# Optimization experiments

Hardware: AMD Instinct MI355X
Metric: run time of the kernel (lower is better)

## Reference

```python
import jax, jax.numpy as jnp
import numpy as np

# norse default LIFParameters (dt=1e-3): tau_mem_inv=100, tau_syn_inv=200, v_leak=0, v_reset=0
DT = 1e-3
TAU_MEM_INV = 100.0
TAU_SYN_INV = 200.0
V_TH_ENC = 1.0   # encoder built with default LIFParameters -> v_th=1.0
V_TH = 0.33      # LIF cells built with v_th=0.33
SEQ_LEN = 24
ALPHA = 100.0    # SuperSpike surrogate-gradient slope (norse 'super' method)

@jax.custom_vjp
def heaviside(x):
    # forward: hard threshold; backward: SuperSpike surrogate 1/(alpha*|x|+1)^2
    return (x > 0).astype(x.dtype)

def _hv_fwd(x):
    return heaviside(x), x

def _hv_bwd(x, g):
    return (g / (ALPHA * jnp.abs(x) + 1.0) ** 2,)

heaviside.defvjp(_hv_fwd, _hv_bwd)


def setup_inputs() -> dict:
    key = jax.random.key(0)
    ks = jax.random.split(key, 6)
    B, F, H, C = 4096, 1024, 256, 10
    def lin(k, fan_out, fan_in):  # torch Linear default init (no bias)
        bound = 1.0 / np.sqrt(fan_in)
        return jax.random.uniform(k, (fan_out, fan_in), jnp.float32, -bound, bound)
    return {
        "x": jax.random.normal(ks[0], (B, F), jnp.float32),
        "W1": lin(ks[1], H, F),
        "W2": lin(ks[2], H, H),
        "W3": lin(ks[3], H, H),
        "Wout": jax.random.normal(ks[4], (C, H), jnp.float32) * np.sqrt(2.0 / H),
        "feature_scalar": jnp.ones((1,), jnp.float32),
        "encoder_scalar": jnp.ones((1,), jnp.float32),
    }


def _lif_step(z_in, v, i):
    # norse lif_feed_forward_step: decay v/i from old state, spike, reset, then inject input into i
    v_dec = v + DT * TAU_MEM_INV * (-v + i)
    i_dec = i * (1.0 - DT * TAU_SYN_INV)
    z = heaviside(v_dec - V_TH)
    v_new = (1.0 - z) * v_dec  # v_reset = 0
    i_new = i_dec + z_in
    return z, v_new, i_new


def reference(x, W1, W2, W3, Wout, feature_scalar, encoder_scalar):
    B, F = x.shape
    H = W1.shape[0]
    C = Wout.shape[0]
    current = 2.0 * feature_scalar * x  # constant injected current, [B, F]
    z0 = lambda d: jnp.zeros((B, d), x.dtype)
    init = (z0(F), z0(H), z0(H), z0(H), z0(H), z0(H), z0(H), z0(C), z0(C))

    def step(state, _):
        v_enc, v1, i1, v2, i2, v3, i3, v_li, i_li = state
        # ConstantCurrentLIFEncoder (lif_current_encoder, v_th=1.0)
        v_enc = v_enc + DT * TAU_MEM_INV * (-v_enc + current)
        s = heaviside(v_enc - V_TH_ENC)
        v_enc = v_enc - s * v_enc  # reset to 0
        z = 5.0 * encoder_scalar * s
        # three Linear(no bias)+LIF stages (dropout in eval mode = identity)
        z, v1, i1 = _lif_step(1.2 * (z @ W1.T), v1, i1)
        z, v2, i2 = _lif_step(1.2 * (z @ W2.T), v2, i2)
        z, v3, i3 = _lif_step(1.2 * (z @ W3.T), v3, i3)
        # LILinearCell: leaky integrator readout
        v_li = v_li + DT * TAU_MEM_INV * (-v_li + i_li)
        i_li = i_li * (1.0 - DT * TAU_SYN_INV) + z @ Wout.T
        return (v_enc, v1, i1, v2, i2, v3, i3, v_li, i_li), None

    final, _ = jax.lax.scan(step, init, None, length=SEQ_LEN)
    return final[7]  # decode = voltages[-1], shape [B, n_classes]
```

## Files before the change

kernel.cpp:

```cpp
#include <hip/hip_runtime.h>

using u16 = unsigned short;
using u32 = unsigned int;
using u64 = unsigned long long;

typedef _Float16 half8 __attribute__((ext_vector_type(8)));
typedef float  f32x4 __attribute__((ext_vector_type(4)));
typedef u32    u32x4 __attribute__((ext_vector_type(4)));
typedef u32    u32x2 __attribute__((ext_vector_type(2)));

#define T_STEPS 24
#define NB 4096
#define NF 1024
#define NH 256
#define NCLS 10

static __device__ __forceinline__ void f16split(float w, u16& hi, u16& lo) {
  _Float16 h = (_Float16)w;
  float hf = (float)h;
  if (__builtin_fabsf(hf) < 6.103515625e-05f) { h = (_Float16)0.0f; hf = 0.0f; }
  float r = __fmul_rn(__fsub_rn(w, hf), 4096.0f);
  _Float16 l = (_Float16)r;
  hi = __builtin_bit_cast(u16, h);
  lo = __builtin_bit_cast(u16, l);
}

__global__ __launch_bounds__(256) void k_prep(const float* __restrict__ W1,
                                              const float* __restrict__ W2,
                                              const float* __restrict__ W3,
                                              u16* __restrict__ W1hl,
                                              u16* __restrict__ W2hl,
                                              u16* __restrict__ W3hl) {
  int blk = blockIdx.x, tid = threadIdx.x;
  const float* src; u16* dst; int K; int g;
  if (blk < 1024)      { src = W1; dst = W1hl; K = 1024; g = blk * 256 + tid; }
  else if (blk < 1280) { src = W2; dst = W2hl; K = 256;  g = (blk - 1024) * 256 + tid; }
  else                 { src = W3; dst = W3hl; K = 256;  g = (blk - 1280) * 256 + tid; }
  int n = g / K, k = g - n * K;
  u16 hi, lo;
  f16split(src[g], hi, lo);
  int p = k >> 6, j = k & 63;
  u16* d = dst + (size_t)n * 2 * K + p * 128 + j;
  d[0] = hi;
  d[64] = lo;
}

template <int NSC, int ASTRIDE>
__device__ __forceinline__ void mega_phase(u16* __restrict__ Bs,
                                           const u32* __restrict__ alds,
                                           const u16* __restrict__ wsrc,
                                           u32* __restrict__ zdst,
                                           float scale,
                                           int wid, int lane, int wm, int wn) {
  constexpr int KTOT = NSC * 64;

  const int bsh   = (lane >> 4) * 8;
  const int rbase = (wn * 64 + (lane & 15)) * 64;
  int pu8[2];
  #pragma unroll
  for (int h = 0; h < 2; ++h)
    pu8[h] = (((4 * h + (lane >> 4)) ^ (lane & 7)) * 8);
  const int sunit = ((lane & 7) ^ (lane >> 3)) * 8;
  const u16* gs = wsrc + (size_t)(wid * 32 + (lane >> 3)) * KTOT + sunit;
  const int ldsw = wid * 2048;

  auto stage = [&](int s, int b) {
    const u16* g = gs + s * 64;
    #pragma unroll
    for (int r = 0; r < 4; ++r)
      __builtin_amdgcn_global_load_lds(
          (const __attribute__((address_space(1))) u32*)(g + (size_t)r * 8 * KTOT),
          (__attribute__((address_space(3))) u32*)&Bs[b * 16384 + ldsw + r * 512],
          16, 0, 0);
  };

  int arow[3];
  #pragma unroll
  for (int ms = 0; ms < 3; ++ms)
    arow[ms] = (wm * 48 + ms * 16 + (lane & 15)) * ASTRIDE;

  auto expand = [&](u32 word) -> half8 {
    u32 by = (word >> bsh) & 0xFFu;
    u32 sp = by * 0x8001u;
    u32x4 d;
    d.x = (sp & 0x10001u) * 0x3C00u;
    d.y = ((sp >> 2) & 0x10001u) * 0x3C00u;
    d.z = ((sp >> 4) & 0x10001u) * 0x3C00u;
    d.w = ((sp >> 6) & 0x10001u) * 0x3C00u;
    return __builtin_bit_cast(half8, d);
  };

  const _Float16 scl = (_Float16)2.44140625e-4f;
  const half8 sc8 = {scl, scl, scl, scl, scl, scl, scl, scl};

  f32x4 acc[3][4];
  #pragma unroll
  for (int ms = 0; ms < 3; ++ms)
    #pragma unroll
    for (int ns = 0; ns < 4; ++ns)
      #pragma unroll
      for (int i = 0; i < 4; ++i) acc[ms][ns][i] = 0.0f;

  stage(0, 0);

  half8 afr[3][2];
  #pragma unroll 2
  for (int s = 0; s < NSC; ++s) {
    __syncthreads();
    if ((s & 1) == 0) {
      u32x2 bw[3];
      #pragma unroll
      for (int ms = 0; ms < 3; ++ms)
        bw[ms] = *(const u32x2*)(alds + arow[ms] + s);
      if (s + 1 < NSC) stage(s + 1, (s + 1) & 1);
      #pragma unroll
      for (int ms = 0; ms < 3; ++ms) {
        afr[ms][0] = expand(bw[ms].x);
        afr[ms][1] = expand(bw[ms].y);
      }
    } else {
      if (s + 1 < NSC) stage(s + 1, (s + 1) & 1);
      #pragma unroll
      for (int ms = 0; ms < 3; ++ms) {
        afr[ms][0] = afr[ms][0] * sc8;
        afr[ms][1] = afr[ms][1] * sc8;
      }
    }

    const int bufo = (s & 1) * 16384;
    __builtin_amdgcn_s_setprio(1);
    #pragma unroll
    for (int h = 0; h < 2; ++h) {
      #pragma unroll
      for (int ns = 0; ns < 4; ++ns) {
        half8 bfr = *(const half8*)&Bs[bufo + rbase + ns * 1024 + pu8[h]];
        #pragma unroll
        for (int ms = 0; ms < 3; ++ms)
          acc[ms][ns] = __builtin_amdgcn_mfma_f32_16x16x32_f16(afr[ms][h], bfr,
                                                               acc[ms][ns], 0, 0, 0);
      }
    }
    __builtin_amdgcn_s_setprio(0);
  }
  __syncthreads();

  float* reg = (float*)Bs + wid * 1600;
  const int q   = lane >> 4, c16 = lane & 15;
  const int b2  = lane >> 5, c   = lane & 31;

  #pragma unroll
  for (int r = 0; r < 2; ++r) {
    #pragma unroll
    for (int ms = 0; ms < 3; ++ms)
      #pragma unroll
      for (int j = 0; j < 2; ++j)
        #pragma unroll
        for (int i = 0; i < 4; ++i)
          reg[(ms * 16 + q * 4 + i) * 33 + j * 16 + c16] =
              __fmul_rn(scale, acc[ms][2 * r + j][i]);
    float v = 0.0f, ii = 0.0f;
    u32 zw = 0;
    #pragma unroll
    for (int t = 0; t < T_STEPS; ++t) {
      float cv = reg[(b2 * 24 + t) * 33 + c];
      float vdec = __fadd_rn(v, __fmul_rn(0.1f, __fsub_rn(ii, v)));
      float idec = __fmul_rn(0.8f, ii);
      bool z = vdec > 0.33f;
      v = z ? 0.0f : vdec;
      ii = __fadd_rn(idec, cv);
      zw |= ((u32)z) << t;
    }
    #pragma unroll
    for (int t = 0; t < T_STEPS; ++t) {
      u64 m = __ballot((zw >> t) & 1u);
      if (c == 0)
        zdst[((wm * 2 + b2) * 24 + t) * 8 + wn * 2 + r] = (u32)(m >> (b2 * 32));
    }
  }
  __syncthreads();
}

__global__ __launch_bounds__(512, 4) void k_mega(const float* __restrict__ x,
                                                 const float* __restrict__ fsp,
                                                 const float* __restrict__ esp,
                                                 const u16* __restrict__ W1hl,
                                                 const u16* __restrict__ W2hl,
                                                 const u16* __restrict__ W3hl,
                                                 const float* __restrict__ Wo,
                                                 float* __restrict__ out) {
  __shared__ __align__(16) u16 Bs[2 * 16384];
  __shared__ u32 zE[96 * 34];
  __shared__ u32 zA[96 * 8];

  const int tid  = threadIdx.x;
  const int wid  = tid >> 6;
  const int lane = tid & 63;
  const int wm   = wid & 1;
  const int wn   = wid >> 1;
  const int b0   = blockIdx.x * 4;

  {
    const int bb = wid >> 1;
    const int fbase = (wid & 1) * 512;
    const float c2 = __fmul_rn(2.0f, fsp[0]);
    float cur[8], v[8];
    #pragma unroll
    for (int j = 0; j < 8; ++j) {
      cur[j] = __fmul_rn(c2, x[(size_t)(b0 + bb) * 1024 + fbase + j * 64 + lane]);
      v[j] = 0.0f;
    }
    #pragma unroll
    for (int t = 0; t < T_STEPS; ++t) {
      #pragma unroll
      for (int j = 0; j < 8; ++j) {
        v[j] = __fadd_rn(v[j], __fmul_rn(0.1f, __fsub_rn(cur[j], v[j])));
        bool s = v[j] > 1.0f;
        if (s) v[j] = 0.0f;
        u64 m = __ballot(s);
        if (lane == 0) {
          int w0 = (bb * 24 + t) * 34 + (fbase >> 5) + 2 * j;
          zE[w0] = (u32)m;
          zE[w0 + 1] = (u32)(m >> 32);
        }
      }
    }
  }
  __syncthreads();

  const float s1 = __fmul_rn(1.2f, __fmul_rn(5.0f, esp[0]));
  mega_phase<32, 34>(Bs, zE, W1hl, zA, s1, wid, lane, wm, wn);
  mega_phase<8, 8>(Bs, zA, W2hl, zE, 1.2f, wid, lane, wm, wn);
  mega_phase<8, 8>(Bs, zE, W3hl, zA, 1.2f, wid, lane, wm, wn);

  {
    float* s_lds = (float*)Bs;
    #pragma unroll
    for (int r = 0; r < 2; ++r) {
      const int idx = tid + r * 512;
      const int b = idx >> 8, h = idx & 255;
      const u32* zp = zA + (b * 24) * 8 + (h >> 5);
      const int bit = h & 31;
      float p9 = 1.0f, p8 = 1.0f, s = 0.0f;
      #pragma unroll
      for (int e = 0; e < 24; ++e) {
        const float a = __fsub_rn(p9, p8);
        const u32 word = zp[(23 - e) * 8];
        s = __fadd_rn(s, ((word >> bit) & 1u) ? a : 0.0f);
        p9 = __fmul_rn(p9, 0.9f);
        p8 = __fmul_rn(p8, 0.8f);
      }
      s_lds[idx] = s;
    }
    __syncthreads();
    #pragma unroll
    for (int oi = 0; oi < 5; ++oi) {
      const int o = wid * 5 + oi;
      const int b = o / 10, cls = o - (o / 10) * 10;
      f32x4 sv = *(const f32x4*)&s_lds[b * 256 + lane * 4];
      f32x4 wv = *(const f32x4*)&Wo[(size_t)cls * 256 + lane * 4];
      float d = __fadd_rn(__fadd_rn(__fmul_rn(sv.x, wv.x), __fmul_rn(sv.y, wv.y)),
                          __fadd_rn(__fmul_rn(sv.z, wv.z), __fmul_rn(sv.w, wv.w)));
      #pragma unroll
      for (int off2 = 32; off2 >= 1; off2 >>= 1)
        d = __fadd_rn(d, __shfl_down(d, off2));
      if (lane == 0) out[(size_t)(b0 + b) * NCLS + cls] = d;
    }
  }
}

extern "C" void kernel_launch(void* const* d_in, const int* in_sizes, int n_in,
                              void* d_out, int out_size, void* d_ws, size_t ws_size,
                              hipStream_t stream) {
  const float* x  = (const float*)d_in[0];
  const float* W1 = (const float*)d_in[1];
  const float* W2 = (const float*)d_in[2];
  const float* W3 = (const float*)d_in[3];
  const float* Wo = (const float*)d_in[4];
  const float* fs = (const float*)d_in[5];
  const float* es = (const float*)d_in[6];

  char* ws = (char*)d_ws;
  const size_t off_w1 = 0;
  const size_t off_w2 = off_w1 + (size_t)NH * 2 * NF * 2;
  const size_t off_w3 = off_w2 + (size_t)NH * 2 * NH * 2;
  const size_t need   = off_w3 + (size_t)NH * 2 * NH * 2;
  if (ws_size < need) return;

  u16* W1hl = (u16*)(ws + off_w1);
  u16* W2hl = (u16*)(ws + off_w2);
  u16* W3hl = (u16*)(ws + off_w3);

  k_prep<<<dim3(1536), dim3(256), 0, stream>>>(W1, W2, W3, W1hl, W2hl, W3hl);
  k_mega<<<dim3(NB / 4), dim3(512), 0, stream>>>(x, fs, es, W1hl, W2hl, W3hl, Wo,
                                                 (float*)d_out);
}
```

Measured before the change: 233.4 us.

## Deepen weight staging to a 4-slot ring with half-size K stages

Splits each 64-wide K chunk of the hi/lo weight stream into two 32-wide stages held in a 4-slot LDS ring, prefetching three stages ahead. A single __syncthreads is replaced by an explicit vmcnt wait plus s_barrier, so the loads stay in flight across iterations. The goal is to hide global-to-LDS latency better while keeping LDS use the same. The cost is twice as many barriers, each with less MFMA work between them. The unswizzled B-fragment layout may also cause LDS bank conflicts.

```diff
diff --git a/kernel.cpp b/kernel.cpp
--- a/kernel.cpp
+++ b/kernel.cpp
@@ -52,27 +52,33 @@
                                            u32* __restrict__ zdst,
                                            float scale,
                                            int wid, int lane, int wm, int wn) {
-  constexpr int KTOT = NSC * 64;
-
-  const int bsh   = (lane >> 4) * 8;
-  const int rbase = (wn * 64 + (lane & 15)) * 64;
-  int pu8[2];
-  #pragma unroll
-  for (int h = 0; h < 2; ++h)
-    pu8[h] = (((4 * h + (lane >> 4)) ^ (lane & 7)) * 8);
-  const int sunit = ((lane & 7) ^ (lane >> 3)) * 8;
-  const u16* gs = wsrc + (size_t)(wid * 32 + (lane >> 3)) * KTOT + sunit;
-  const int ldsw = wid * 2048;
-
-  auto stage = [&](int s, int b) {
-    const u16* g = gs + s * 64;
-    #pragma unroll
-    for (int r = 0; r < 4; ++r)
+  constexpr int KTOT = NSC * 32;
+  constexpr int NG   = NSC / 4;
+
+  const int q   = lane >> 4;
+  const int bsh = q * 8;
+
+  const u16* gs = wsrc + (size_t)(wid * 32 + (lane >> 2)) * KTOT + (lane & 3) * 8;
+  const int sdst = wid * 1024;
+
+  auto stage = [&](int s) {
+    const int slot = s & 3;
+    const u16* g = gs + s * 32;
+    #pragma unroll
+    for (int r = 0; r < 2; ++r)
       __builtin_amdgcn_global_load_lds(
-          (const __attribute__((address_space(1))) u32*)(g + (size_t)r * 8 * KTOT),
-          (__attribute__((address_space(3))) u32*)&Bs[b * 16384 + ldsw + r * 512],
+          (const __attribute__((address_space(1))) u32*)(g + (size_t)r * 16 * KTOT),
+          (__attribute__((address_space(3))) u32*)&Bs[slot * 8192 + sdst + r * 512],
           16, 0, 0);
   };
+
+  auto waitv = [&](int n) {
+    if (n == 4)      asm volatile("s_waitcnt vmcnt(4)" ::: "memory");
+    else if (n == 2) asm volatile("s_waitcnt vmcnt(2)" ::: "memory");
+    else             asm volatile("s_waitcnt vmcnt(0)" ::: "memory");
+  };
+
+  const int bru = (wn * 64 + (lane & 15)) * 32 + q * 8;
 
   int arow[3];
   #pragma unroll
@@ -101,52 +107,64 @@
       #pragma unroll
       for (int i = 0; i < 4; ++i) acc[ms][ns][i] = 0.0f;
 
-  stage(0, 0);
-
   half8 afr[3][2];
-  #pragma unroll 2
-  for (int s = 0; s < NSC; ++s) {
-    __syncthreads();
-    if ((s & 1) == 0) {
-      u32x2 bw[3];
-      #pragma unroll
-      for (int ms = 0; ms < 3; ++ms)
-        bw[ms] = *(const u32x2*)(alds + arow[ms] + s);
-      if (s + 1 < NSC) stage(s + 1, (s + 1) & 1);
+
+  auto body = [&](int s, int j, int wcnt, bool dostage) {
+    waitv(wcnt);
+    __builtin_amdgcn_s_barrier();
+    asm volatile("" ::: "memory");
+    if (dostage) stage(s + 3);
+    if (j == 0) {
       #pragma unroll
       for (int ms = 0; ms < 3; ++ms) {
-        afr[ms][0] = expand(bw[ms].x);
-        afr[ms][1] = expand(bw[ms].y);
+        u32x2 bw = *(const u32x2*)(alds + arow[ms] + (s >> 2) * 2);
+        afr[ms][0] = expand(bw.x);
+        afr[ms][1] = expand(bw.y);
       }
-    } else {
-      if (s + 1 < NSC) stage(s + 1, (s + 1) & 1);
+    } else if (j == 2) {
       #pragma unroll
       for (int ms = 0; ms < 3; ++ms) {
         afr[ms][0] = afr[ms][0] * sc8;
         afr[ms][1] = afr[ms][1] * sc8;
       }
     }
-
-    const int bufo = (s & 1) * 16384;
+    const int sel  = j & 1;
+    const int slot = s & 3;
+    half8 bfr[4];
+    #pragma unroll
+    for (int ns = 0; ns < 4; ++ns)
+      bfr[ns] = *(const half8*)&Bs[slot * 8192 + bru + ns * 512];
     __builtin_amdgcn_s_setprio(1);
     #pragma unroll
-    for (int h = 0; h < 2; ++h) {
-      #pragma unroll
-      for (int ns = 0; ns < 4; ++ns) {
-        half8 bfr = *(const half8*)&Bs[bufo + rbase + ns * 1024 + pu8[h]];
-        #pragma unroll
-        for (int ms = 0; ms < 3; ++ms)
-          acc[ms][ns] = __builtin_amdgcn_mfma_f32_16x16x32_f16(afr[ms][h], bfr,
-                                                               acc[ms][ns], 0, 0, 0);
-      }
-    }
+    for (int ns = 0; ns < 4; ++ns)
+      #pragma unroll
+      for (int ms = 0; ms < 3; ++ms)
+        acc[ms][ns] = __builtin_amdgcn_mfma_f32_16x16x32_f16(afr[ms][sel], bfr[ns],
+                                                             acc[ms][ns], 0, 0, 0);
     __builtin_amdgcn_s_setprio(0);
+  };
+
+  stage(0); stage(1); stage(2);
+
+  #pragma unroll 2
+  for (int g = 0; g < NG - 1; ++g) {
+    body(4 * g + 0, 0, 4, true);
+    body(4 * g + 1, 1, 4, true);
+    body(4 * g + 2, 2, 4, true);
+    body(4 * g + 3, 3, 4, true);
+  }
+  {
+    const int g = NG - 1;
+    body(4 * g + 0, 0, 4, true);
+    body(4 * g + 1, 1, 4, false);
+    body(4 * g + 2, 2, 2, false);
+    body(4 * g + 3, 3, 0, false);
   }
   __syncthreads();
 
   float* reg = (float*)Bs + wid * 1600;
-  const int q   = lane >> 4, c16 = lane & 15;
-  const int b2  = lane >> 5, c   = lane & 31;
+  const int c16 = lane & 15;
+  const int b2  = lane >> 5, c = lane & 31;
 
   #pragma unroll
   for (int r = 0; r < 2; ++r) {
@@ -188,7 +206,7 @@
                                                  const u16* __restrict__ W3hl,
                                                  const float* __restrict__ Wo,
                                                  float* __restrict__ out) {
-  __shared__ __align__(16) u16 Bs[2 * 16384];
+  __shared__ __align__(16) u16 Bs[4 * 8192];
   __shared__ u32 zE[96 * 34];
   __shared__ u32 zA[96 * 8];
 
@@ -228,9 +246,9 @@
   __syncthreads();
 
   const float s1 = __fmul_rn(1.2f, __fmul_rn(5.0f, esp[0]));
-  mega_phase<32, 34>(Bs, zE, W1hl, zA, s1, wid, lane, wm, wn);
-  mega_phase<8, 8>(Bs, zA, W2hl, zE, 1.2f, wid, lane, wm, wn);
-  mega_phase<8, 8>(Bs, zE, W3hl, zA, 1.2f, wid, lane, wm, wn);
+  mega_phase<64, 34>(Bs, zE, W1hl, zA, s1, wid, lane, wm, wn);
+  mega_phase<16, 8>(Bs, zA, W2hl, zE, 1.2f, wid, lane, wm, wn);
+  mega_phase<16, 8>(Bs, zE, W3hl, zA, 1.2f, wid, lane, wm, wn);
 
   {
     float* s_lds = (float*)Bs;
```

After: 246.2 us. 1.05x slower.

## Double batch rows per block to reuse each staged weight tile twice

Applied to the files above, without the earlier changes.

Each block now handles 8 batch samples (192 time-rows) instead of 4, so every weight tile staged into LDS feeds six M-subtiles per wave instead of three. This halves the number of blocks and the total weight traffic from global/L2 into LDS. The LIF epilogue and the bit-packing of spikes are reworked for 16-column chunks with 16-bit ballot writes. In exchange, accumulator registers double and occupancy drops (launch bounds go from 4 to 2 blocks per CU), and larger LDS spike buffers may limit how many blocks fit.

```diff
diff --git a/kernel.cpp b/kernel.cpp
--- a/kernel.cpp
+++ b/kernel.cpp
@@ -54,12 +54,14 @@
                                            int wid, int lane, int wm, int wn) {
   constexpr int KTOT = NSC * 64;
 
-  const int bsh   = (lane >> 4) * 8;
-  const int rbase = (wn * 64 + (lane & 15)) * 64;
+  const int q    = lane >> 4;
+  const int bsh  = q * 8;
+  const int c16  = lane & 15;
+  const int rbase = (wn * 64 + c16) * 64;
   int pu8[2];
   #pragma unroll
   for (int h = 0; h < 2; ++h)
-    pu8[h] = (((4 * h + (lane >> 4)) ^ (lane & 7)) * 8);
+    pu8[h] = (((4 * h + q) ^ (lane & 7)) * 8);
   const int sunit = ((lane & 7) ^ (lane >> 3)) * 8;
   const u16* gs = wsrc + (size_t)(wid * 32 + (lane >> 3)) * KTOT + sunit;
   const int ldsw = wid * 2048;
@@ -74,10 +76,10 @@
           16, 0, 0);
   };
 
-  int arow[3];
-  #pragma unroll
-  for (int ms = 0; ms < 3; ++ms)
-    arow[ms] = (wm * 48 + ms * 16 + (lane & 15)) * ASTRIDE;
+  int arow[6];
+  #pragma unroll
+  for (int ms = 0; ms < 6; ++ms)
+    arow[ms] = (wm * 96 + ms * 16 + c16) * ASTRIDE;
 
   auto expand = [&](u32 word) -> half8 {
     u32 by = (word >> bsh) & 0xFFu;
@@ -93,9 +95,9 @@
   const _Float16 scl = (_Float16)2.44140625e-4f;
   const half8 sc8 = {scl, scl, scl, scl, scl, scl, scl, scl};
 
-  f32x4 acc[3][4];
-  #pragma unroll
-  for (int ms = 0; ms < 3; ++ms)
+  f32x4 acc[6][4];
+  #pragma unroll
+  for (int ms = 0; ms < 6; ++ms)
     #pragma unroll
     for (int ns = 0; ns < 4; ++ns)
       #pragma unroll
@@ -103,25 +105,25 @@
 
   stage(0, 0);
 
-  half8 afr[3][2];
+  half8 afr[6][2];
   #pragma unroll 2
   for (int s = 0; s < NSC; ++s) {
     __syncthreads();
     if ((s & 1) == 0) {
-      u32x2 bw[3];
-      #pragma unroll
-      for (int ms = 0; ms < 3; ++ms)
+      u32x2 bw[6];
+      #pragma unroll
+      for (int ms = 0; ms < 6; ++ms)
         bw[ms] = *(const u32x2*)(alds + arow[ms] + s);
       if (s + 1 < NSC) stage(s + 1, (s + 1) & 1);
       #pragma unroll
-      for (int ms = 0; ms < 3; ++ms) {
+      for (int ms = 0; ms < 6; ++ms) {
         afr[ms][0] = expand(bw[ms].x);
         afr[ms][1] = expand(bw[ms].y);
       }
     } else {
       if (s + 1 < NSC) stage(s + 1, (s + 1) & 1);
       #pragma unroll
-      for (int ms = 0; ms < 3; ++ms) {
+      for (int ms = 0; ms < 6; ++ms) {
         afr[ms][0] = afr[ms][0] * sc8;
         afr[ms][1] = afr[ms][1] * sc8;
       }
@@ -135,7 +137,7 @@
       for (int ns = 0; ns < 4; ++ns) {
         half8 bfr = *(const half8*)&Bs[bufo + rbase + ns * 1024 + pu8[h]];
         #pragma unroll
-        for (int ms = 0; ms < 3; ++ms)
+        for (int ms = 0; ms < 6; ++ms)
           acc[ms][ns] = __builtin_amdgcn_mfma_f32_16x16x32_f16(afr[ms][h], bfr,
                                                                acc[ms][ns], 0, 0, 0);
       }
@@ -144,25 +146,20 @@
   }
   __syncthreads();
 
-  float* reg = (float*)Bs + wid * 1600;
-  const int q   = lane >> 4, c16 = lane & 15;
-  const int b2  = lane >> 5, c   = lane & 31;
-
-  #pragma unroll
-  for (int r = 0; r < 2; ++r) {
-    #pragma unroll
-    for (int ms = 0; ms < 3; ++ms)
-      #pragma unroll
-      for (int j = 0; j < 2; ++j)
-        #pragma unroll
-        for (int i = 0; i < 4; ++i)
-          reg[(ms * 16 + q * 4 + i) * 33 + j * 16 + c16] =
-              __fmul_rn(scale, acc[ms][2 * r + j][i]);
+  float* reg = (float*)Bs + wid * 1632;
+
+  #pragma unroll
+  for (int r = 0; r < 4; ++r) {
+    #pragma unroll
+    for (int ms = 0; ms < 6; ++ms)
+      #pragma unroll
+      for (int i = 0; i < 4; ++i)
+        reg[(ms * 16 + q * 4 + i) * 17 + c16] = __fmul_rn(scale, acc[ms][r][i]);
     float v = 0.0f, ii = 0.0f;
     u32 zw = 0;
     #pragma unroll
     for (int t = 0; t < T_STEPS; ++t) {
-      float cv = reg[(b2 * 24 + t) * 33 + c];
+      float cv = reg[(q * 24 + t) * 17 + c16];
       float vdec = __fadd_rn(v, __fmul_rn(0.1f, __fsub_rn(ii, v)));
       float idec = __fmul_rn(0.8f, ii);
       bool z = vdec > 0.33f;
@@ -173,14 +170,16 @@
     #pragma unroll
     for (int t = 0; t < T_STEPS; ++t) {
       u64 m = __ballot((zw >> t) & 1u);
-      if (c == 0)
-        zdst[((wm * 2 + b2) * 24 + t) * 8 + wn * 2 + r] = (u32)(m >> (b2 * 32));
+      if (c16 == 0) {
+        u16 val = (u16)(m >> (q * 16));
+        ((u16*)&zdst[((wm * 4 + q) * 24 + t) * 8 + wn * 2 + (r >> 1)])[r & 1] = val;
+      }
     }
   }
   __syncthreads();
 }
 
-__global__ __launch_bounds__(512, 4) void k_mega(const float* __restrict__ x,
+__global__ __launch_bounds__(512, 2) void k_mega(const float* __restrict__ x,
                                                  const float* __restrict__ fsp,
                                                  const float* __restrict__ esp,
                                                  const u16* __restrict__ W1hl,
@@ -189,36 +188,34 @@
                                                  const float* __restrict__ Wo,
                                                  float* __restrict__ out) {
   __shared__ __align__(16) u16 Bs[2 * 16384];
-  __shared__ u32 zE[96 * 34];
-  __shared__ u32 zA[96 * 8];
+  __shared__ u32 zE[192 * 34];
+  __shared__ u32 zA[192 * 8];
 
   const int tid  = threadIdx.x;
   const int wid  = tid >> 6;
   const int lane = tid & 63;
   const int wm   = wid & 1;
   const int wn   = wid >> 1;
-  const int b0   = blockIdx.x * 4;
+  const int b0   = blockIdx.x * 8;
 
   {
-    const int bb = wid >> 1;
-    const int fbase = (wid & 1) * 512;
     const float c2 = __fmul_rn(2.0f, fsp[0]);
-    float cur[8], v[8];
-    #pragma unroll
-    for (int j = 0; j < 8; ++j) {
-      cur[j] = __fmul_rn(c2, x[(size_t)(b0 + bb) * 1024 + fbase + j * 64 + lane]);
+    float cur[16], v[16];
+    #pragma unroll
+    for (int j = 0; j < 16; ++j) {
+      cur[j] = __fmul_rn(c2, x[(size_t)(b0 + wid) * 1024 + j * 64 + lane]);
       v[j] = 0.0f;
     }
     #pragma unroll
     for (int t = 0; t < T_STEPS; ++t) {
       #pragma unroll
-      for (int j = 0; j < 8; ++j) {
+      for (int j = 0; j < 16; ++j) {
         v[j] = __fadd_rn(v[j], __fmul_rn(0.1f, __fsub_rn(cur[j], v[j])));
         bool s = v[j] > 1.0f;
         if (s) v[j] = 0.0f;
         u64 m = __ballot(s);
         if (lane == 0) {
-          int w0 = (bb * 24 + t) * 34 + (fbase >> 5) + 2 * j;
+          int w0 = (wid * 24 + t) * 34 + 2 * j;
           zE[w0] = (u32)m;
           zE[w0 + 1] = (u32)(m >> 32);
         }
@@ -235,7 +232,7 @@
   {
     float* s_lds = (float*)Bs;
     #pragma unroll
-    for (int r = 0; r < 2; ++r) {
+    for (int r = 0; r < 4; ++r) {
       const int idx = tid + r * 512;
       const int b = idx >> 8, h = idx & 255;
       const u32* zp = zA + (b * 24) * 8 + (h >> 5);
@@ -253,17 +250,15 @@
     }
     __syncthreads();
     #pragma unroll
-    for (int oi = 0; oi < 5; ++oi) {
-      const int o = wid * 5 + oi;
-      const int b = o / 10, cls = o - (o / 10) * 10;
-      f32x4 sv = *(const f32x4*)&s_lds[b * 256 + lane * 4];
+    for (int cls = 0; cls < NCLS; ++cls) {
+      f32x4 sv = *(const f32x4*)&s_lds[wid * 256 + lane * 4];
       f32x4 wv = *(const f32x4*)&Wo[(size_t)cls * 256 + lane * 4];
       float d = __fadd_rn(__fadd_rn(__fmul_rn(sv.x, wv.x), __fmul_rn(sv.y, wv.y)),
                           __fadd_rn(__fmul_rn(sv.z, wv.z), __fmul_rn(sv.w, wv.w)));
       #pragma unroll
       for (int off2 = 32; off2 >= 1; off2 >>= 1)
         d = __fadd_rn(d, __shfl_down(d, off2));
-      if (lane == 0) out[(size_t)(b0 + b) * NCLS + cls] = d;
+      if (lane == 0) out[(size_t)(b0 + wid) * NCLS + cls] = d;
     }
   }
 }
@@ -291,6 +286,6 @@
   u16* W3hl = (u16*)(ws + off_w3);
 
   k_prep<<<dim3(1536), dim3(256), 0, stream>>>(W1, W2, W3, W1hl, W2hl, W3hl);
-  k_mega<<<dim3(NB / 4), dim3(512), 0, stream>>>(x, fs, es, W1hl, W2hl, W3hl, Wo,
+  k_mega<<<dim3(NB / 8), dim3(512), 0, stream>>>(x, fs, es, W1hl, W2hl, W3hl, Wo,
                                                  (float*)d_out);
 }
```

Measured after the change: 265.1 us. +13.6%, slower.
